# Kernel tuning notes

Measured on AMD Instinct MI355X. Metric: run time of the kernel, lower is better.

The kernel has to match this reference:

```python
import jax, jax.numpy as jnp
import numpy as np

BETA = 0.25

def setup_inputs() -> dict:
    key = jax.random.key(0)
    k1, k2 = jax.random.split(key)
    N, D, K = 262144, 64, 512
    encoding = jax.random.normal(k1, (N, D), dtype=jnp.float32)
    # original inits uniform(-1/K, 1/K); scale a normal similarly is fine, but stay faithful:
    weight = jax.random.uniform(k2, (K, D), dtype=jnp.float32, minval=-1.0 / K, maxval=1.0 / K)
    return {"encoding": encoding, "weight": weight}


def reference(encoding, weight):
    # flat view: encoding already [N, D]
    x = encoding  # [N, D]
    # squared euclidean distances; argmin is invariant to sqrt and to ||x||^2 term
    x2 = jnp.sum(x * x, axis=1, keepdims=True)            # [N, 1]
    w2 = jnp.sum(weight * weight, axis=1)                  # [K]
    d2 = x2 - 2.0 * (x @ weight.T) + w2[None, :]           # [N, K]
    idx = jnp.argmin(d2, axis=1)                           # [N]
    quantized = weight[idx]                                # gather == one_hot @ weight, [N, D]

    commitment_loss = jnp.mean((jax.lax.stop_gradient(quantized) - x) ** 2)
    embedding_loss = jnp.mean((quantized - jax.lax.stop_gradient(x)) ** 2)
    vq_loss = commitment_loss * BETA + embedding_loss

    # straight-through estimator
    quantized_st = x + jax.lax.stop_gradient(quantized - x)
    return (idx[:, None], quantized_st, vq_loss)
```

## Files before the change

### kernel.cpp

```cpp
#include <hip/hip_runtime.h>

#define NROWS 262144
#define DDIM  64
#define KCB   512

#define MARGKEY (3u << 17)

#define WS_CNT   0
#define WS_W2P3  1024
#define WS_WHI   4096
#define WS_WMID  69632
#define WS_LIST  135168

typedef __attribute__((ext_vector_type(8))) short short8;
typedef __attribute__((ext_vector_type(4))) float floatx4;
typedef __attribute__((ext_vector_type(16))) float floatx16;
typedef __attribute__((ext_vector_type(2))) unsigned int uintx2;

#if defined(__has_builtin)
#if __has_builtin(__builtin_amdgcn_permlane32_swap)
#define VQ_PLSWAP 1
#endif
#endif

__device__ __forceinline__ unsigned umin2(unsigned a, unsigned b) { return a < b ? a : b; }
__device__ __forceinline__ unsigned umax2(unsigned a, unsigned b) { return a > b ? a : b; }

__device__ __forceinline__ float np_sumsq64(const float* a) {
    float r[8];
#pragma unroll
    for (int j = 0; j < 8; ++j) r[j] = __fmul_rn(a[j], a[j]);
#pragma unroll
    for (int i = 8; i < 64; i += 8) {
#pragma unroll
        for (int j = 0; j < 8; ++j)
            r[j] = __fadd_rn(r[j], __fmul_rn(a[i + j], a[i + j]));
    }
    return __fadd_rn(__fadd_rn(__fadd_rn(r[0], r[1]), __fadd_rn(r[2], r[3])),
                     __fadd_rn(__fadd_rn(r[4], r[5]), __fadd_rn(r[6], r[7])));
}

__device__ __forceinline__ void split2(float e0, float e1, unsigned& hid, unsigned& mid) {
    unsigned u0 = __float_as_uint(e0), u1 = __float_as_uint(e1);
    float r0 = __fsub_rn(e0, __uint_as_float(u0 & 0xFFFF0000u));
    float r1 = __fsub_rn(e1, __uint_as_float(u1 & 0xFFFF0000u));
    hid = (u0 >> 16) | (u1 & 0xFFFF0000u);
    mid = (__float_as_uint(r0) >> 16) | (__float_as_uint(r1) & 0xFFFF0000u);
}

__device__ __forceinline__ void split4(float4 v, uint2& h, uint2& m) {
    unsigned h0, m0, h1, m1;
    split2(v.x, v.y, h0, m0);
    split2(v.z, v.w, h1, m1);
    h = make_uint2(h0, h1);
    m = make_uint2(m0, m1);
}

__device__ __forceinline__ void merge32(unsigned& m1, unsigned& m2) {
#ifdef VQ_PLSWAP
    uintx2 s1 = __builtin_amdgcn_permlane32_swap(m1, m1, false, false);
    uintx2 s2 = __builtin_amdgcn_permlane32_swap(m2, m2, false, false);
    m2 = umin2(umin2(s2[0], s2[1]), umax2(s1[0], s1[1]));
    m1 = umin2(s1[0], s1[1]);
#else
    unsigned o1 = __shfl_xor((int)m1, 32);
    unsigned o2 = __shfl_xor((int)m2, 32);
    m2 = umin2(umin2(m2, o2), umax2(m1, o1));
    m1 = umin2(m1, o1);
#endif
}

__device__ __forceinline__ void top2_16(const unsigned* k, unsigned& m1, unsigned& m2) {
    unsigned lo[8], hi[8];
#pragma unroll
    for (int i = 0; i < 8; ++i) {
        lo[i] = umin2(k[2 * i], k[2 * i + 1]);
        hi[i] = umax2(k[2 * i], k[2 * i + 1]);
    }
#pragma unroll
    for (int s = 4; s >= 1; s >>= 1) {
#pragma unroll
        for (int i = 0; i < s; ++i) {
            unsigned l = umin2(lo[i], lo[i + s]);
            unsigned h = umin2(umax2(lo[i], lo[i + s]), umin2(hi[i], hi[i + s]));
            lo[i] = l; hi[i] = h;
        }
    }
    m1 = lo[0]; m2 = hi[0];
}

__global__ void vq_prep(const float* __restrict__ w, float* __restrict__ w2p3,
                        unsigned short* __restrict__ whi,
                        unsigned short* __restrict__ wmid,
                        unsigned* __restrict__ cnt, float* __restrict__ loss) {
    const int k = blockIdx.x * blockDim.x + threadIdx.x;
    if (k == 0) { *cnt = 0u; *loss = 0.0f; }
    float ws[64];
    const float4* wp = (const float4*)(w + (size_t)k * DDIM);
#pragma unroll
    for (int j = 0; j < 16; ++j) {
        float4 v = wp[j];
        ws[4 * j + 0] = v.x; ws[4 * j + 1] = v.y;
        ws[4 * j + 2] = v.z; ws[4 * j + 3] = v.w;
    }
    w2p3[k] = __fadd_rn(np_sumsq64(ws), 3.0f);
#pragma unroll
    for (int j = 0; j < 8; ++j) {
        union { unsigned d[4]; short8 s; } H, M;
#pragma unroll
        for (int t = 0; t < 4; ++t) {
            float v0 = __fmul_rn(-2.0f, ws[8 * j + 2 * t]);
            float v1 = __fmul_rn(-2.0f, ws[8 * j + 2 * t + 1]);
            split2(v0, v1, H.d[t], M.d[t]);
        }
        *(short8*)(whi  + (size_t)k * 64 + 8 * j) = H.s;
        *(short8*)(wmid + (size_t)k * 64 + 8 * j) = M.s;
    }
}

__launch_bounds__(256, 4)
__global__ void vq_gemm(const float* __restrict__ x,
                        const unsigned short* __restrict__ whi,
                        const unsigned short* __restrict__ wmid,
                        const float* __restrict__ w2p3g,
                        uint2* __restrict__ mmg) {
    const int tid = threadIdx.x;
    const int wave = tid >> 6, lane = tid & 63;
    const int row32 = lane & 31;
    const int khalf = lane >> 5;
    const int half = blockIdx.x & 1;
    const int r0 = (blockIdx.x >> 1) * 256;

    __shared__ float w2p3s[256];
    __shared__ __align__(16) unsigned sbh[2][32 * 36];
    __shared__ __align__(16) unsigned sbm[2][32 * 36];
    __shared__ uint2 mm[4][8][32];

    w2p3s[tid] = w2p3g[half * 256 + tid];

    short8 ah[2][4], am[2][4];
#pragma unroll
    for (int tt = 0; tt < 2; ++tt) {
        const size_t cw = (size_t)(half * 256 + wave * 64 + tt * 32 + row32);
#pragma unroll
        for (int t = 0; t < 4; ++t) {
            const size_t off = cw * 64 + t * 16 + khalf * 8;
            ah[tt][t] = *(const short8*)(whi + off);
            am[tt][t] = *(const short8*)(wmid + off);
        }
    }

    const int srow = tid >> 4, sc4 = tid & 15;
    {
        float4 v0 = *(const float4*)(x + (size_t)(r0 + srow) * DDIM + 4 * sc4);
        float4 v1 = *(const float4*)(x + (size_t)(r0 + srow + 16) * DDIM + 4 * sc4);
        uint2 h, m;
        split4(v0, h, m);
        *(uint2*)&sbh[0][srow * 36 + 2 * sc4] = h;
        *(uint2*)&sbm[0][srow * 36 + 2 * sc4] = m;
        split4(v1, h, m);
        *(uint2*)&sbh[0][(srow + 16) * 36 + 2 * sc4] = h;
        *(uint2*)&sbm[0][(srow + 16) * 36 + 2 * sc4] = m;
    }
    __syncthreads();

    const unsigned cwk = (unsigned)(half * 256 + wave * 64 + 4 * khalf);

    for (int it = 0; it < 8; ++it) {
        const int p = it & 1;
        float4 pre0, pre1;
        if (it < 7) {
            pre0 = *(const float4*)(x + (size_t)(r0 + (it + 1) * 32 + srow) * DDIM + 4 * sc4);
            pre1 = *(const float4*)(x + (size_t)(r0 + (it + 1) * 32 + srow + 16) * DDIM + 4 * sc4);
        }

        short8 bh[4], bm[4];
#pragma unroll
        for (int t = 0; t < 4; ++t) {
            bh[t] = *(const short8*)&sbh[p][row32 * 36 + t * 8 + khalf * 4];
            bm[t] = *(const short8*)&sbm[p][row32 * 36 + t * 8 + khalf * 4];
        }

        unsigned r1t[2], r2t[2];
#pragma unroll
        for (int tt = 0; tt < 2; ++tt) {
            floatx16 acc;
            const int wb = wave * 64 + tt * 32 + 4 * khalf;
#pragma unroll
            for (int g = 0; g < 4; ++g) {
                floatx4 v = *(const floatx4*)&w2p3s[wb + 8 * g];
                acc[4 * g + 0] = v[0]; acc[4 * g + 1] = v[1];
                acc[4 * g + 2] = v[2]; acc[4 * g + 3] = v[3];
            }
#pragma unroll
            for (int t = 0; t < 4; ++t) {
                acc = __builtin_amdgcn_mfma_f32_32x32x16_bf16(ah[tt][t], bh[t], acc, 0, 0, 0);
                acc = __builtin_amdgcn_mfma_f32_32x32x16_bf16(ah[tt][t], bm[t], acc, 0, 0, 0);
                acc = __builtin_amdgcn_mfma_f32_32x32x16_bf16(am[tt][t], bh[t], acc, 0, 0, 0);
            }
            unsigned keys[16];
#pragma unroll
            for (int r = 0; r < 16; ++r) {
                const unsigned moff = (unsigned)((r & 3) + 8 * (r >> 2) + tt * 32);
                keys[r] = (__float_as_uint(acc[r]) << 9) + cwk + moff;
            }
            top2_16(keys, r1t[tt], r2t[tt]);
        }
        unsigned m1 = umin2(r1t[0], r1t[1]);
        unsigned m2 = umin2(umax2(r1t[0], r1t[1]), umin2(r2t[0], r2t[1]));
        merge32(m1, m2);
        if (lane < 32) mm[wave][it][row32] = make_uint2(m1, m2);

        if (it < 7) {
            uint2 h, m;
            split4(pre0, h, m);
            *(uint2*)&sbh[p ^ 1][srow * 36 + 2 * sc4] = h;
            *(uint2*)&sbm[p ^ 1][srow * 36 + 2 * sc4] = m;
            split4(pre1, h, m);
            *(uint2*)&sbh[p ^ 1][(srow + 16) * 36 + 2 * sc4] = h;
            *(uint2*)&sbm[p ^ 1][(srow + 16) * 36 + 2 * sc4] = m;
        }
        __syncthreads();
    }

    unsigned a1 = 0xFFFFFFFFu, a2 = 0xFFFFFFFFu;
#pragma unroll
    for (int wv = 0; wv < 4; ++wv) {
        uint2 v = mm[wv][tid >> 5][tid & 31];
        a2 = umin2(umin2(a2, v.y), umax2(a1, v.x));
        a1 = umin2(a1, v.x);
    }
    mmg[(size_t)half * NROWS + (r0 + tid)] = make_uint2(a1, a2);
}

__launch_bounds__(256)
__global__ void vq_merge(const uint2* __restrict__ mmg,
                         float* __restrict__ out_idx,
                         unsigned* __restrict__ cnt,
                         unsigned* __restrict__ list, int listcap) {
    const int row = blockIdx.x * 256 + threadIdx.x;
    const int lane = threadIdx.x & 63;
    uint2 v0 = mmg[row];
    uint2 v1 = mmg[(size_t)NROWS + row];
    unsigned a1 = umin2(v0.x, v1.x);
    unsigned a2 = umin2(umax2(v0.x, v1.x), umin2(v0.y, v1.y));
    out_idx[row] = (float)(a1 & 511u);
    bool flag = (a2 - a1 < MARGKEY);
    unsigned long long mask = __ballot(flag);
    int nw = __popcll(mask);
    unsigned base = 0;
    if (lane == 0 && nw) base = atomicAdd(cnt, (unsigned)nw);
    base = (unsigned)__shfl((int)base, 0);
    if (flag) {
        unsigned pos = base + (unsigned)__popcll(mask & ((1ull << lane) - 1ull));
        if ((int)pos < listcap) list[pos] = (unsigned)row;
    }
}

__launch_bounds__(512, 4)
__global__ void vq_recheck(const float* __restrict__ x,
                           const float* __restrict__ w,
                           const unsigned* __restrict__ cnt,
                           const unsigned* __restrict__ list, int listcap,
                           float* __restrict__ out_idx) {
    const int tid = threadIdx.x;
    unsigned total = *cnt;
    if (total > (unsigned)listcap) total = (unsigned)listcap;
    const unsigned nb = (total + 15) >> 4;
    if (blockIdx.x >= nb) return;

    float wl[64];
    {
        const float4* wp = (const float4*)(w + (size_t)tid * DDIM);
#pragma unroll
        for (int j = 0; j < 16; ++j) {
            float4 v = wp[j];
            wl[4 * j + 0] = v.x; wl[4 * j + 1] = v.y;
            wl[4 * j + 2] = v.z; wl[4 * j + 3] = v.w;
        }
    }
    const float w2l = np_sumsq64(wl);

    __shared__ float d2tile[16][KCB];
    __shared__ int rowbuf[16];
    __shared__ float x2buf[16];

    for (unsigned batch = blockIdx.x; batch < nb; batch += gridDim.x) {
        if (tid < 16) {
            unsigned li = batch * 16 + (unsigned)tid;
            rowbuf[tid] = (li < total) ? (int)list[li] : -1;
        }
        __syncthreads();

        if (tid < 128) {
            const int rl = tid >> 3, j = tid & 7;
            int row = rowbuf[rl]; if (row < 0) row = 0;
            const float* xr = x + (size_t)row * DDIM;
            float a0 = xr[j];
            float r = __fmul_rn(a0, a0);
#pragma unroll
            for (int i = 1; i < 8; ++i) {
                float ai = xr[8 * i + j];
                r = __fadd_rn(r, __fmul_rn(ai, ai));
            }
            float s1 = __fadd_rn(r,  __shfl_xor(r, 1));
            float s2 = __fadd_rn(s1, __shfl_xor(s1, 2));
            float s4 = __fadd_rn(s2, __shfl_xor(s2, 4));
            if (j == 0) x2buf[rl] = s4;
        }
        __syncthreads();

        for (int g = 0; g < 16; g += 4) {
            int ra = rowbuf[g + 0]; if (ra < 0) ra = 0;
            int rb = rowbuf[g + 1]; if (rb < 0) rb = 0;
            int rc = rowbuf[g + 2]; if (rc < 0) rc = 0;
            int rd = rowbuf[g + 3]; if (rd < 0) rd = 0;
            const float* xr0 = x + (size_t)ra * DDIM;
            const float* xr1 = x + (size_t)rb * DDIM;
            const float* xr2 = x + (size_t)rc * DDIM;
            const float* xr3 = x + (size_t)rd * DDIM;
            float m0 = 0.f, m1 = 0.f, m2 = 0.f, m3 = 0.f;
#pragma unroll
            for (int jb = 0; jb < 16; ++jb) {
                float4 a0 = *(const float4*)(xr0 + 4 * jb);
                float4 a1 = *(const float4*)(xr1 + 4 * jb);
                float4 a2 = *(const float4*)(xr2 + 4 * jb);
                float4 a3 = *(const float4*)(xr3 + 4 * jb);
                m0 = __fmaf_rn(a0.x, wl[4 * jb + 0], m0);
                m0 = __fmaf_rn(a0.y, wl[4 * jb + 1], m0);
                m0 = __fmaf_rn(a0.z, wl[4 * jb + 2], m0);
                m0 = __fmaf_rn(a0.w, wl[4 * jb + 3], m0);
                m1 = __fmaf_rn(a1.x, wl[4 * jb + 0], m1);
                m1 = __fmaf_rn(a1.y, wl[4 * jb + 1], m1);
                m1 = __fmaf_rn(a1.z, wl[4 * jb + 2], m1);
                m1 = __fmaf_rn(a1.w, wl[4 * jb + 3], m1);
                m2 = __fmaf_rn(a2.x, wl[4 * jb + 0], m2);
                m2 = __fmaf_rn(a2.y, wl[4 * jb + 1], m2);
                m2 = __fmaf_rn(a2.z, wl[4 * jb + 2], m2);
                m2 = __fmaf_rn(a2.w, wl[4 * jb + 3], m2);
                m3 = __fmaf_rn(a3.x, wl[4 * jb + 0], m3);
                m3 = __fmaf_rn(a3.y, wl[4 * jb + 1], m3);
                m3 = __fmaf_rn(a3.z, wl[4 * jb + 2], m3);
                m3 = __fmaf_rn(a3.w, wl[4 * jb + 3], m3);
            }
            float X0 = x2buf[g + 0], X1 = x2buf[g + 1];
            float X2 = x2buf[g + 2], X3 = x2buf[g + 3];
            d2tile[g + 0][tid] = __fadd_rn(__fsub_rn(X0, __fmul_rn(2.0f, m0)), w2l);
            d2tile[g + 1][tid] = __fadd_rn(__fsub_rn(X1, __fmul_rn(2.0f, m1)), w2l);
            d2tile[g + 2][tid] = __fadd_rn(__fsub_rn(X2, __fmul_rn(2.0f, m2)), w2l);
            d2tile[g + 3][tid] = __fadd_rn(__fsub_rn(X3, __fmul_rn(2.0f, m3)), w2l);
        }
        __syncthreads();

        {
            const int rl  = tid >> 5;
            const int sub = tid & 31;
            float bv = d2tile[rl][sub];
            int   bi = sub;
#pragma unroll
            for (int i = 1; i < 16; ++i) {
                int cc = sub + 32 * i;
                float v = d2tile[rl][cc];
                if (v < bv) { bv = v; bi = cc; }
            }
#pragma unroll
            for (int s = 1; s < 32; s <<= 1) {
                float ov = __shfl_xor(bv, s);
                int   oi = __shfl_xor(bi, s);
                if (ov < bv || (ov == bv && oi < bi)) { bv = ov; bi = oi; }
            }
            if (sub == 0 && rowbuf[rl] >= 0) out_idx[rowbuf[rl]] = (float)bi;
        }
        __syncthreads();
    }
}

__launch_bounds__(256)
__global__ void vq_epilogue(const float* __restrict__ x,
                            const float* __restrict__ w,
                            const float* __restrict__ out_idx_f,
                            float* __restrict__ out_q,
                            float* __restrict__ out_loss) {
    const int tid = threadIdx.x;
    const int r0  = blockIdx.x * 256;
    const int bidx = (int)out_idx_f[r0 + tid];
    const float4* wq = (const float4*)(w + (size_t)bidx * DDIM);

    __shared__ float tile[128][65];
    __shared__ float red[4];

    float ls = 0.0f;
#pragma unroll
    for (int ph = 0; ph < 2; ++ph) {
        const int rb = r0 + ph * 128;
        __syncthreads();
#pragma unroll
        for (int i = 0; i < 8; ++i) {
            const int li = tid + 256 * i;
            const int row = li >> 4, c4 = li & 15;
            float4 v = *(const float4*)(x + (size_t)(rb + row) * DDIM + 4 * c4);
            *(float4*)&tile[row][4 * c4] = v;
        }
        __syncthreads();
        if ((tid >> 7) == ph) {
            const int lr = tid & 127;
#pragma unroll
            for (int j = 0; j < 16; ++j) {
                float4 xv = *(const float4*)&tile[lr][4 * j];
                float4 wv = wq[j];
                float e0 = __fsub_rn(wv.x, xv.x), e1 = __fsub_rn(wv.y, xv.y);
                float e2 = __fsub_rn(wv.z, xv.z), e3 = __fsub_rn(wv.w, xv.w);
                ls = fmaf(e0, e0, ls); ls = fmaf(e1, e1, ls);
                ls = fmaf(e2, e2, ls); ls = fmaf(e3, e3, ls);
                float4 q;
                q.x = __fadd_rn(xv.x, e0); q.y = __fadd_rn(xv.y, e1);
                q.z = __fadd_rn(xv.z, e2); q.w = __fadd_rn(xv.w, e3);
                *(float4*)&tile[lr][4 * j] = q;
            }
        }
        __syncthreads();
#pragma unroll
        for (int i = 0; i < 8; ++i) {
            const int li = tid + 256 * i;
            const int row = li >> 4, c4 = li & 15;
            float4 qv = *(const float4*)&tile[row][4 * c4];
            *(float4*)(out_q + (size_t)(rb + row) * DDIM + 4 * c4) = qv;
        }
    }

#pragma unroll
    for (int off = 32; off > 0; off >>= 1) ls += __shfl_down(ls, off);
    const int lane = tid & 63;
    const int wid  = tid >> 6;
    if (lane == 0) red[wid] = ls;
    __syncthreads();
    if (tid == 0) {
        float t = (red[0] + red[1]) + (red[2] + red[3]);
        atomicAdd(out_loss, t * (1.25f / (float)(NROWS * DDIM)));
    }
}

extern "C" void kernel_launch(void* const* d_in, const int* in_sizes, int n_in,
                              void* d_out, int out_size, void* d_ws, size_t ws_size,
                              hipStream_t stream) {
    const float* x = (const float*)d_in[0];
    const float* w = (const float*)d_in[1];

    float* out      = (float*)d_out;
    float* out_idx  = out;
    float* out_q    = out + (size_t)NROWS;
    float* out_loss = out + (size_t)NROWS + (size_t)NROWS * DDIM;

    uint2* mmg = (uint2*)out_q;

    char* ws = (char*)d_ws;
    unsigned* cnt  = (unsigned*)(ws + WS_CNT);
    float* w2p3    = (float*)(ws + WS_W2P3);
    unsigned short* whi  = (unsigned short*)(ws + WS_WHI);
    unsigned short* wmid = (unsigned short*)(ws + WS_WMID);
    unsigned* list = (unsigned*)(ws + WS_LIST);
    long cap = ((long)ws_size - WS_LIST) / 4;
    int listcap = cap > 0 ? (cap > NROWS ? NROWS : (int)cap) : 0;

    vq_prep<<<2, 256, 0, stream>>>(w, w2p3, whi, wmid, cnt, out_loss);
    vq_gemm<<<2048, 256, 0, stream>>>(x, whi, wmid, w2p3, mmg);
    vq_merge<<<NROWS / 256, 256, 0, stream>>>(mmg, out_idx, cnt, list, listcap);
    vq_recheck<<<256, 512, 0, stream>>>(x, w, cnt, list, listcap, out_idx);
    vq_epilogue<<<NROWS / 256, 256, 0, stream>>>(x, w, out_idx, out_q, out_loss);
}
```

Baseline: 248.5 us.

## Fold codebook prep into GEMM and fuse merge+recheck via cooperative launch

Drops the separate prep kernel: each GEMM block now computes codebook norms and the hi/mid bf16 split directly from the fp32 weights. The merge and recheck kernels become one cooperative kernel that uses a grid sync between building the candidate list and rechecking it. Block indices are remapped so the two codebook halves for neighbouring row units run close together. This removes two kernel launches, but every GEMM block now repeats the prep arithmetic, and the grid-wide sync plus 256-thread recheck blocks add their own overhead.

```diff
diff --git a/kernel.cpp b/kernel.cpp
--- a/kernel.cpp
+++ b/kernel.cpp
@@ -1,4 +1,7 @@
 #include <hip/hip_runtime.h>
+#include <hip/hip_cooperative_groups.h>
+
+namespace cg = cooperative_groups;
 
 #define NROWS 262144
 #define DDIM  64
@@ -7,9 +10,6 @@
 #define MARGKEY (3u << 17)
 
 #define WS_CNT   0
-#define WS_W2P3  1024
-#define WS_WHI   4096
-#define WS_WMID  69632
 #define WS_LIST  135168
 
 typedef __attribute__((ext_vector_type(8))) short short8;
@@ -35,6 +35,30 @@
 #pragma unroll
         for (int j = 0; j < 8; ++j)
             r[j] = __fadd_rn(r[j], __fmul_rn(a[i + j], a[i + j]));
+    }
+    return __fadd_rn(__fadd_rn(__fadd_rn(r[0], r[1]), __fadd_rn(r[2], r[3])),
+                     __fadd_rn(__fadd_rn(r[4], r[5]), __fadd_rn(r[6], r[7])));
+}
+
+__device__ __forceinline__ float np_sumsq64_stream(const float* a) {
+    const float4* p = (const float4*)a;
+    float4 v0 = p[0], v1 = p[1];
+    float r[8];
+    r[0] = __fmul_rn(v0.x, v0.x); r[1] = __fmul_rn(v0.y, v0.y);
+    r[2] = __fmul_rn(v0.z, v0.z); r[3] = __fmul_rn(v0.w, v0.w);
+    r[4] = __fmul_rn(v1.x, v1.x); r[5] = __fmul_rn(v1.y, v1.y);
+    r[6] = __fmul_rn(v1.z, v1.z); r[7] = __fmul_rn(v1.w, v1.w);
+#pragma unroll
+    for (int i = 1; i < 8; ++i) {
+        float4 u0 = p[2 * i], u1 = p[2 * i + 1];
+        r[0] = __fadd_rn(r[0], __fmul_rn(u0.x, u0.x));
+        r[1] = __fadd_rn(r[1], __fmul_rn(u0.y, u0.y));
+        r[2] = __fadd_rn(r[2], __fmul_rn(u0.z, u0.z));
+        r[3] = __fadd_rn(r[3], __fmul_rn(u0.w, u0.w));
+        r[4] = __fadd_rn(r[4], __fmul_rn(u1.x, u1.x));
+        r[5] = __fadd_rn(r[5], __fmul_rn(u1.y, u1.y));
+        r[6] = __fadd_rn(r[6], __fmul_rn(u1.z, u1.z));
+        r[7] = __fadd_rn(r[7], __fmul_rn(u1.w, u1.w));
     }
     return __fadd_rn(__fadd_rn(__fadd_rn(r[0], r[1]), __fadd_rn(r[2], r[3])),
                      __fadd_rn(__fadd_rn(r[4], r[5]), __fadd_rn(r[6], r[7])));
@@ -54,6 +78,15 @@
     split2(v.z, v.w, h1, m1);
     h = make_uint2(h0, h1);
     m = make_uint2(m0, m1);
+}
+
+__device__ __forceinline__ void build8n2(float4 a, float4 b, short8& hi, short8& mi) {
+    union { unsigned d[4]; short8 s; } H, M;
+    split2(__fmul_rn(-2.0f, a.x), __fmul_rn(-2.0f, a.y), H.d[0], M.d[0]);
+    split2(__fmul_rn(-2.0f, a.z), __fmul_rn(-2.0f, a.w), H.d[1], M.d[1]);
+    split2(__fmul_rn(-2.0f, b.x), __fmul_rn(-2.0f, b.y), H.d[2], M.d[2]);
+    split2(__fmul_rn(-2.0f, b.z), __fmul_rn(-2.0f, b.w), H.d[3], M.d[3]);
+    hi = H.s; mi = M.s;
 }
 
 __device__ __forceinline__ void merge32(unsigned& m1, unsigned& m2) {
@@ -89,54 +122,29 @@
     m1 = lo[0]; m2 = hi[0];
 }
 
-__global__ void vq_prep(const float* __restrict__ w, float* __restrict__ w2p3,
-                        unsigned short* __restrict__ whi,
-                        unsigned short* __restrict__ wmid,
-                        unsigned* __restrict__ cnt, float* __restrict__ loss) {
-    const int k = blockIdx.x * blockDim.x + threadIdx.x;
-    if (k == 0) { *cnt = 0u; *loss = 0.0f; }
-    float ws[64];
-    const float4* wp = (const float4*)(w + (size_t)k * DDIM);
-#pragma unroll
-    for (int j = 0; j < 16; ++j) {
-        float4 v = wp[j];
-        ws[4 * j + 0] = v.x; ws[4 * j + 1] = v.y;
-        ws[4 * j + 2] = v.z; ws[4 * j + 3] = v.w;
-    }
-    w2p3[k] = __fadd_rn(np_sumsq64(ws), 3.0f);
-#pragma unroll
-    for (int j = 0; j < 8; ++j) {
-        union { unsigned d[4]; short8 s; } H, M;
-#pragma unroll
-        for (int t = 0; t < 4; ++t) {
-            float v0 = __fmul_rn(-2.0f, ws[8 * j + 2 * t]);
-            float v1 = __fmul_rn(-2.0f, ws[8 * j + 2 * t + 1]);
-            split2(v0, v1, H.d[t], M.d[t]);
-        }
-        *(short8*)(whi  + (size_t)k * 64 + 8 * j) = H.s;
-        *(short8*)(wmid + (size_t)k * 64 + 8 * j) = M.s;
-    }
-}
-
 __launch_bounds__(256, 4)
 __global__ void vq_gemm(const float* __restrict__ x,
-                        const unsigned short* __restrict__ whi,
-                        const unsigned short* __restrict__ wmid,
-                        const float* __restrict__ w2p3g,
-                        uint2* __restrict__ mmg) {
+                        const float* __restrict__ w,
+                        uint2* __restrict__ mmg,
+                        unsigned* __restrict__ cnt,
+                        float* __restrict__ loss) {
     const int tid = threadIdx.x;
+    const int bid = blockIdx.x;
+    if (bid == 0 && tid == 0) { *cnt = 0u; *loss = 0.0f; }
+
     const int wave = tid >> 6, lane = tid & 63;
     const int row32 = lane & 31;
     const int khalf = lane >> 5;
-    const int half = blockIdx.x & 1;
-    const int r0 = (blockIdx.x >> 1) * 256;
+    const int half = (bid >> 3) & 1;
+    const int unit = (bid & 7) | ((bid >> 4) << 3);
+    const int r0 = unit * 256;
 
     __shared__ float w2p3s[256];
     __shared__ __align__(16) unsigned sbh[2][32 * 36];
     __shared__ __align__(16) unsigned sbm[2][32 * 36];
     __shared__ uint2 mm[4][8][32];
 
-    w2p3s[tid] = w2p3g[half * 256 + tid];
+    w2p3s[tid] = __fadd_rn(np_sumsq64_stream(w + (size_t)(half * 256 + tid) * DDIM), 3.0f);
 
     short8 ah[2][4], am[2][4];
 #pragma unroll
@@ -144,9 +152,10 @@
         const size_t cw = (size_t)(half * 256 + wave * 64 + tt * 32 + row32);
 #pragma unroll
         for (int t = 0; t < 4; ++t) {
-            const size_t off = cw * 64 + t * 16 + khalf * 8;
-            ah[tt][t] = *(const short8*)(whi + off);
-            am[tt][t] = *(const short8*)(wmid + off);
+            const float* wp = w + cw * 64 + t * 16 + khalf * 8;
+            float4 a = *(const float4*)wp;
+            float4 b = *(const float4*)(wp + 4);
+            build8n2(a, b, ah[tt][t], am[tt][t]);
         }
     }
 
@@ -233,59 +242,49 @@
     mmg[(size_t)half * NROWS + (r0 + tid)] = make_uint2(a1, a2);
 }
 
-__launch_bounds__(256)
-__global__ void vq_merge(const uint2* __restrict__ mmg,
-                         float* __restrict__ out_idx,
-                         unsigned* __restrict__ cnt,
-                         unsigned* __restrict__ list, int listcap) {
-    const int row = blockIdx.x * 256 + threadIdx.x;
-    const int lane = threadIdx.x & 63;
-    uint2 v0 = mmg[row];
-    uint2 v1 = mmg[(size_t)NROWS + row];
-    unsigned a1 = umin2(v0.x, v1.x);
-    unsigned a2 = umin2(umax2(v0.x, v1.x), umin2(v0.y, v1.y));
-    out_idx[row] = (float)(a1 & 511u);
-    bool flag = (a2 - a1 < MARGKEY);
-    unsigned long long mask = __ballot(flag);
-    int nw = __popcll(mask);
-    unsigned base = 0;
-    if (lane == 0 && nw) base = atomicAdd(cnt, (unsigned)nw);
-    base = (unsigned)__shfl((int)base, 0);
-    if (flag) {
-        unsigned pos = base + (unsigned)__popcll(mask & ((1ull << lane) - 1ull));
-        if ((int)pos < listcap) list[pos] = (unsigned)row;
-    }
-}
-
-__launch_bounds__(512, 4)
-__global__ void vq_recheck(const float* __restrict__ x,
-                           const float* __restrict__ w,
-                           const unsigned* __restrict__ cnt,
-                           const unsigned* __restrict__ list, int listcap,
-                           float* __restrict__ out_idx) {
+__launch_bounds__(256, 4)
+__global__ void vq_tail(const float* __restrict__ x,
+                        const float* __restrict__ w,
+                        const uint2* __restrict__ mmg,
+                        float* __restrict__ out_idx,
+                        unsigned* __restrict__ cnt,
+                        unsigned* __restrict__ list, int listcap) {
+    cg::grid_group grid = cg::this_grid();
     const int tid = threadIdx.x;
+    const int bid = blockIdx.x;
+    const int lane = tid & 63;
+
+#pragma unroll
+    for (int c = 0; c < 2; ++c) {
+        const int row = bid * 512 + c * 256 + tid;
+        uint2 v0 = mmg[row];
+        uint2 v1 = mmg[(size_t)NROWS + row];
+        unsigned a1 = umin2(v0.x, v1.x);
+        unsigned a2 = umin2(umax2(v0.x, v1.x), umin2(v0.y, v1.y));
+        out_idx[row] = (float)(a1 & 511u);
+        bool flag = (a2 - a1 < MARGKEY);
+        unsigned long long mask = __ballot(flag);
+        int nw = __popcll(mask);
+        unsigned base = 0;
+        if (lane == 0 && nw) base = atomicAdd(cnt, (unsigned)nw);
+        base = (unsigned)__shfl((int)base, 0);
+        if (flag) {
+            unsigned pos = base + (unsigned)__popcll(mask & ((1ull << lane) - 1ull));
+            if ((int)pos < listcap) list[pos] = (unsigned)row;
+        }
+    }
+    __threadfence();
+    grid.sync();
+
     unsigned total = *cnt;
     if (total > (unsigned)listcap) total = (unsigned)listcap;
     const unsigned nb = (total + 15) >> 4;
-    if (blockIdx.x >= nb) return;
-
-    float wl[64];
-    {
-        const float4* wp = (const float4*)(w + (size_t)tid * DDIM);
-#pragma unroll
-        for (int j = 0; j < 16; ++j) {
-            float4 v = wp[j];
-            wl[4 * j + 0] = v.x; wl[4 * j + 1] = v.y;
-            wl[4 * j + 2] = v.z; wl[4 * j + 3] = v.w;
-        }
-    }
-    const float w2l = np_sumsq64(wl);
 
     __shared__ float d2tile[16][KCB];
     __shared__ int rowbuf[16];
     __shared__ float x2buf[16];
 
-    for (unsigned batch = blockIdx.x; batch < nb; batch += gridDim.x) {
+    for (unsigned batch = (unsigned)bid; batch < nb; batch += 512u) {
         if (tid < 16) {
             unsigned li = batch * 16 + (unsigned)tid;
             rowbuf[tid] = (li < total) ? (int)list[li] : -1;
@@ -310,61 +309,77 @@
         }
         __syncthreads();
 
-        for (int g = 0; g < 16; g += 4) {
-            int ra = rowbuf[g + 0]; if (ra < 0) ra = 0;
-            int rb = rowbuf[g + 1]; if (rb < 0) rb = 0;
-            int rc = rowbuf[g + 2]; if (rc < 0) rc = 0;
-            int rd = rowbuf[g + 3]; if (rd < 0) rd = 0;
-            const float* xr0 = x + (size_t)ra * DDIM;
-            const float* xr1 = x + (size_t)rb * DDIM;
-            const float* xr2 = x + (size_t)rc * DDIM;
-            const float* xr3 = x + (size_t)rd * DDIM;
-            float m0 = 0.f, m1 = 0.f, m2 = 0.f, m3 = 0.f;
-#pragma unroll
-            for (int jb = 0; jb < 16; ++jb) {
-                float4 a0 = *(const float4*)(xr0 + 4 * jb);
-                float4 a1 = *(const float4*)(xr1 + 4 * jb);
-                float4 a2 = *(const float4*)(xr2 + 4 * jb);
-                float4 a3 = *(const float4*)(xr3 + 4 * jb);
-                m0 = __fmaf_rn(a0.x, wl[4 * jb + 0], m0);
-                m0 = __fmaf_rn(a0.y, wl[4 * jb + 1], m0);
-                m0 = __fmaf_rn(a0.z, wl[4 * jb + 2], m0);
-                m0 = __fmaf_rn(a0.w, wl[4 * jb + 3], m0);
-                m1 = __fmaf_rn(a1.x, wl[4 * jb + 0], m1);
-                m1 = __fmaf_rn(a1.y, wl[4 * jb + 1], m1);
-                m1 = __fmaf_rn(a1.z, wl[4 * jb + 2], m1);
-                m1 = __fmaf_rn(a1.w, wl[4 * jb + 3], m1);
-                m2 = __fmaf_rn(a2.x, wl[4 * jb + 0], m2);
-                m2 = __fmaf_rn(a2.y, wl[4 * jb + 1], m2);
-                m2 = __fmaf_rn(a2.z, wl[4 * jb + 2], m2);
-                m2 = __fmaf_rn(a2.w, wl[4 * jb + 3], m2);
-                m3 = __fmaf_rn(a3.x, wl[4 * jb + 0], m3);
-                m3 = __fmaf_rn(a3.y, wl[4 * jb + 1], m3);
-                m3 = __fmaf_rn(a3.z, wl[4 * jb + 2], m3);
-                m3 = __fmaf_rn(a3.w, wl[4 * jb + 3], m3);
-            }
-            float X0 = x2buf[g + 0], X1 = x2buf[g + 1];
-            float X2 = x2buf[g + 2], X3 = x2buf[g + 3];
-            d2tile[g + 0][tid] = __fadd_rn(__fsub_rn(X0, __fmul_rn(2.0f, m0)), w2l);
-            d2tile[g + 1][tid] = __fadd_rn(__fsub_rn(X1, __fmul_rn(2.0f, m1)), w2l);
-            d2tile[g + 2][tid] = __fadd_rn(__fsub_rn(X2, __fmul_rn(2.0f, m2)), w2l);
-            d2tile[g + 3][tid] = __fadd_rn(__fsub_rn(X3, __fmul_rn(2.0f, m3)), w2l);
+#pragma unroll 1
+        for (int pass = 0; pass < 2; ++pass) {
+            const int mycw = pass * 256 + tid;
+            float wl[64];
+            {
+                const float4* wp = (const float4*)(w + (size_t)mycw * DDIM);
+#pragma unroll
+                for (int j = 0; j < 16; ++j) {
+                    float4 v = wp[j];
+                    wl[4 * j + 0] = v.x; wl[4 * j + 1] = v.y;
+                    wl[4 * j + 2] = v.z; wl[4 * j + 3] = v.w;
+                }
+            }
+            const float w2l = np_sumsq64(wl);
+
+            for (int g = 0; g < 16; g += 4) {
+                int ra = rowbuf[g + 0]; if (ra < 0) ra = 0;
+                int rb = rowbuf[g + 1]; if (rb < 0) rb = 0;
+                int rc = rowbuf[g + 2]; if (rc < 0) rc = 0;
+                int rd = rowbuf[g + 3]; if (rd < 0) rd = 0;
+                const float* xr0 = x + (size_t)ra * DDIM;
+                const float* xr1 = x + (size_t)rb * DDIM;
+                const float* xr2 = x + (size_t)rc * DDIM;
+                const float* xr3 = x + (size_t)rd * DDIM;
+                float m0 = 0.f, m1 = 0.f, m2 = 0.f, m3 = 0.f;
+#pragma unroll
+                for (int jb = 0; jb < 16; ++jb) {
+                    float4 a0 = *(const float4*)(xr0 + 4 * jb);
+                    float4 a1 = *(const float4*)(xr1 + 4 * jb);
+                    float4 a2 = *(const float4*)(xr2 + 4 * jb);
+                    float4 a3 = *(const float4*)(xr3 + 4 * jb);
+                    m0 = __fmaf_rn(a0.x, wl[4 * jb + 0], m0);
+                    m0 = __fmaf_rn(a0.y, wl[4 * jb + 1], m0);
+                    m0 = __fmaf_rn(a0.z, wl[4 * jb + 2], m0);
+                    m0 = __fmaf_rn(a0.w, wl[4 * jb + 3], m0);
+                    m1 = __fmaf_rn(a1.x, wl[4 * jb + 0], m1);
+                    m1 = __fmaf_rn(a1.y, wl[4 * jb + 1], m1);
+                    m1 = __fmaf_rn(a1.z, wl[4 * jb + 2], m1);
+                    m1 = __fmaf_rn(a1.w, wl[4 * jb + 3], m1);
+                    m2 = __fmaf_rn(a2.x, wl[4 * jb + 0], m2);
+                    m2 = __fmaf_rn(a2.y, wl[4 * jb + 1], m2);
+                    m2 = __fmaf_rn(a2.z, wl[4 * jb + 2], m2);
+                    m2 = __fmaf_rn(a2.w, wl[4 * jb + 3], m2);
+                    m3 = __fmaf_rn(a3.x, wl[4 * jb + 0], m3);
+                    m3 = __fmaf_rn(a3.y, wl[4 * jb + 1], m3);
+                    m3 = __fmaf_rn(a3.z, wl[4 * jb + 2], m3);
+                    m3 = __fmaf_rn(a3.w, wl[4 * jb + 3], m3);
+                }
+                float X0 = x2buf[g + 0], X1 = x2buf[g + 1];
+                float X2 = x2buf[g + 2], X3 = x2buf[g + 3];
+                d2tile[g + 0][mycw] = __fadd_rn(__fsub_rn(X0, __fmul_rn(2.0f, m0)), w2l);
+                d2tile[g + 1][mycw] = __fadd_rn(__fsub_rn(X1, __fmul_rn(2.0f, m1)), w2l);
+                d2tile[g + 2][mycw] = __fadd_rn(__fsub_rn(X2, __fmul_rn(2.0f, m2)), w2l);
+                d2tile[g + 3][mycw] = __fadd_rn(__fsub_rn(X3, __fmul_rn(2.0f, m3)), w2l);
+            }
         }
         __syncthreads();
 
         {
-            const int rl  = tid >> 5;
-            const int sub = tid & 31;
+            const int rl  = tid >> 4;
+            const int sub = tid & 15;
             float bv = d2tile[rl][sub];
             int   bi = sub;
 #pragma unroll
-            for (int i = 1; i < 16; ++i) {
-                int cc = sub + 32 * i;
+            for (int i = 1; i < 32; ++i) {
+                int cc = sub + 16 * i;
                 float v = d2tile[rl][cc];
                 if (v < bv) { bv = v; bi = cc; }
             }
 #pragma unroll
-            for (int s = 1; s < 32; s <<= 1) {
+            for (int s = 1; s < 16; s <<= 1) {
                 float ov = __shfl_xor(bv, s);
                 int   oi = __shfl_xor(bi, s);
                 if (ov < bv || (ov == bv && oi < bi)) { bv = ov; bi = oi; }
@@ -455,16 +470,20 @@
 
     char* ws = (char*)d_ws;
     unsigned* cnt  = (unsigned*)(ws + WS_CNT);
-    float* w2p3    = (float*)(ws + WS_W2P3);
-    unsigned short* whi  = (unsigned short*)(ws + WS_WHI);
-    unsigned short* wmid = (unsigned short*)(ws + WS_WMID);
     unsigned* list = (unsigned*)(ws + WS_LIST);
     long cap = ((long)ws_size - WS_LIST) / 4;
     int listcap = cap > 0 ? (cap > NROWS ? NROWS : (int)cap) : 0;
 
-    vq_prep<<<2, 256, 0, stream>>>(w, w2p3, whi, wmid, cnt, out_loss);
-    vq_gemm<<<2048, 256, 0, stream>>>(x, whi, wmid, w2p3, mmg);
-    vq_merge<<<NROWS / 256, 256, 0, stream>>>(mmg, out_idx, cnt, list, listcap);
-    vq_recheck<<<256, 512, 0, stream>>>(x, w, cnt, list, listcap, out_idx);
+    vq_gemm<<<2048, 256, 0, stream>>>(x, w, mmg, cnt, out_loss);
+
+    {
+        const float* xx = x; const float* ww = w;
+        const uint2* mm = mmg; float* oi = out_idx;
+        unsigned* cp = cnt; unsigned* lp = list; int lc = listcap;
+        void* args[] = { &xx, &ww, &mm, &oi, &cp, &lp, &lc };
+        hipLaunchCooperativeKernel((const void*)vq_tail, dim3(512), dim3(256),
+                                   args, 0, stream);
+    }
+
     vq_epilogue<<<NROWS / 256, 256, 0, stream>>>(x, w, out_idx, out_q, out_loss);
 }
```

Result: slower. 345.9 us (+39.2%).
